# Kernel tuning notes

Measured on AMD Instinct MI355X. Metric: run time of the kernel, lower is better.

Reference implementation:

```python
import jax, jax.numpy as jnp
import numpy as np
import math

B, T, S, C, E = 8, 2048, 2048, 1024, 1024

def setup_inputs() -> dict:
    key = jax.random.key(0)
    ks = jax.random.split(key, 6)
    x = jax.random.normal(ks[0], (B, T, C), dtype=jnp.float32)
    tgt = jax.random.normal(ks[1], (B, T, E), dtype=jnp.float32)
    enc_a = jax.random.normal(ks[2], (B, E, S), dtype=jnp.float32)
    enc_b = jax.random.normal(ks[3], (B, S, E), dtype=jnp.float32)
    mask = jax.random.randint(ks[4], (B, S), 0, 2).astype(bool)
    w_in = jax.random.normal(ks[5], (E, C), dtype=jnp.float32) * math.sqrt(1.0 / C)
    b_in = jnp.zeros((E,), dtype=jnp.float32)
    w_out = jax.random.normal(jax.random.fold_in(key, 7), (C, E), dtype=jnp.float32) * math.sqrt(1.0 / E)
    b_out = jnp.zeros((C,), dtype=jnp.float32)
    return {"x": x, "target_embedding": tgt, "encoder_a": enc_a, "encoder_b": enc_b,
            "encoder_padding_mask": mask, "w_in": w_in, "b_in": b_in,
            "w_out": w_out, "b_out": b_out}

def reference(x, target_embedding, encoder_a, encoder_b, encoder_padding_mask,
              w_in, b_in, w_out, b_out):
    residual = x
    h = (jnp.einsum('btc,ec->bte', x, w_in) + b_in + target_embedding) * math.sqrt(0.5)
    # attention scores: [B, T, S]
    scores = jnp.einsum('bte,bes->bts', h, encoder_a)
    scores = jnp.where(encoder_padding_mask[:, None, :], -jnp.inf, scores)
    attn = jax.nn.softmax(scores, axis=-1)
    out = jnp.einsum('bts,bse->bte', attn, encoder_b)
    s = encoder_b.shape[1]
    out = out * (s * math.sqrt(1.0 / s))
    out = (jnp.einsum('bte,ce->btc', out, w_out) + b_out + residual) * math.sqrt(0.5)
    return (out, attn)
```

## Files before the change

kernel.cpp:

```cpp
#include <hip/hip_runtime.h>
#include <hip/hip_bf16.h>
#include <math.h>

#define NB 8
#define TT 2048
#define SS 2048
#define CC 1024
#define EE 1024
#define NMAX 1280

typedef __attribute__((ext_vector_type(8))) short short8;
typedef __attribute__((ext_vector_type(4))) float f32x4;

__device__ __forceinline__ unsigned short f2bf(float f) {
  unsigned u = __builtin_bit_cast(unsigned, f);
  u += 0x7fffu + ((u >> 16) & 1u);
  return (unsigned short)(u >> 16);
}
__device__ __forceinline__ float bf2f(unsigned short h) {
  unsigned u = ((unsigned)h) << 16;
  return __builtin_bit_cast(float, u);
}
__device__ __forceinline__ void gload16(const void* g, void* l) {
  __builtin_amdgcn_global_load_lds((const __attribute__((address_space(1))) void*)g,
                                   (__attribute__((address_space(3))) void*)l, 16, 0, 0);
}
__device__ __forceinline__ unsigned ldsoff(const void* p) {
  return (unsigned)(size_t)(const __attribute__((address_space(3))) char*)p;
}
__device__ __forceinline__ short8 ds128(unsigned off) {
  short8 r;
  asm volatile("ds_read_b128 %0, %1" : "=v"(r) : "v"(off));
  return r;
}
__device__ __forceinline__ int swzi(int x) { return x ^ (((x >> 7) & 7) << 4); }

#define WAITV(N) asm volatile("s_waitcnt vmcnt(" #N ")" ::: "memory")
#define WAITL(N) asm volatile("s_waitcnt lgkmcnt(" #N ")" ::: "memory")
#define BAR() __builtin_amdgcn_s_barrier()
#define SCH0() __builtin_amdgcn_sched_barrier(0)
#define PRIO1() __builtin_amdgcn_s_setprio(1)
#define PRIO0() __builtin_amdgcn_s_setprio(0)
#define MF(a_, b_, c_) __builtin_amdgcn_mfma_f32_16x16x32_bf16(a_, b_, c_, 0, 0, 0)

__device__ __forceinline__ int xcd_logical() {
  int gx = gridDim.x, gy = gridDim.y, gz = gridDim.z;
  int pid = blockIdx.x + gx * (blockIdx.y + gy * blockIdx.z);
  int q = (gx * gy * gz) >> 3;
  return (pid & 7) * q + (pid >> 3);
}

__global__ __launch_bounds__(256) void k_scan(const int* __restrict__ mask,
    int* __restrict__ idx, int* __restrict__ pfx, int* __restrict__ cnt,
    int* __restrict__ kpad) {
  __shared__ int cs[256];
  int b = blockIdx.x, t = threadIdx.x;
  const int* mrow = mask + (size_t)b * SS;
  int4 a = ((const int4*)mrow)[t * 2];
  int4 c2 = ((const int4*)mrow)[t * 2 + 1];
  int mm[8] = {a.x, a.y, a.z, a.w, c2.x, c2.y, c2.z, c2.w};
  int c = 0;
#pragma unroll
  for (int j = 0; j < 8; ++j) c += (mm[j] == 0);
  cs[t] = c;
  __syncthreads();
  if (t == 0) {
    int run = 0;
    for (int i = 0; i < 256; ++i) { int tmp = cs[i]; cs[i] = run; run += tmp; }
    cnt[b] = run;
    int kp = (run + 127) & ~127;
    if (kp > NMAX) kp = NMAX;
    kpad[b] = kp;
  }
  __syncthreads();
  int base = cs[t];
#pragma unroll
  for (int j = 0; j < 8; ++j) {
    int s = t * 8 + j;
    pfx[(size_t)b * SS + s] = base;
    if (mm[j] == 0) { idx[(size_t)b * SS + base] = s; base++; }
  }
}

__global__ __launch_bounds__(256) void k_split(const float* __restrict__ in,
    unsigned short* __restrict__ hi, unsigned short* __restrict__ lo, long n4) {
  long i = (long)blockIdx.x * blockDim.x + threadIdx.x;
  long stride = (long)gridDim.x * blockDim.x;
  for (; i < n4; i += stride) {
    float4 v = ((const float4*)in)[i];
    float f[4] = {v.x, v.y, v.z, v.w};
    unsigned short hh[4], ll[4];
#pragma unroll
    for (int j = 0; j < 4; ++j) {
      hh[j] = f2bf(f[j]);
      ll[j] = f2bf(f[j] - bf2f(hh[j]));
    }
    ushort4 h; h.x = hh[0]; h.y = hh[1]; h.z = hh[2]; h.w = hh[3];
    ushort4 l; l.x = ll[0]; l.y = ll[1]; l.z = ll[2]; l.w = ll[3];
    ((ushort4*)hi)[i] = h;
    ((ushort4*)lo)[i] = l;
  }
}

__global__ __launch_bounds__(256) void k_conv(const float* __restrict__ in,
    unsigned short* __restrict__ out, long n4) {
  long i = (long)blockIdx.x * blockDim.x + threadIdx.x;
  long stride = (long)gridDim.x * blockDim.x;
  for (; i < n4; i += stride) {
    float4 v = ((const float4*)in)[i];
    ushort4 h; h.x = f2bf(v.x); h.y = f2bf(v.y); h.z = f2bf(v.z); h.w = f2bf(v.w);
    ((ushort4*)out)[i] = h;
  }
}

__global__ __launch_bounds__(256) void k_ta(const float* __restrict__ enca,
    const int* __restrict__ idx, const int* __restrict__ cnt,
    unsigned short* __restrict__ hi, unsigned short* __restrict__ lo) {
  __shared__ float tile[64][65];
  int b = blockIdx.z, sc0 = blockIdx.x * 64, e0 = blockIdx.y * 64;
  int cb = cnt[b];
  const float* src = enca + (size_t)b * EE * SS;
  int t = threadIdx.x, tr = t >> 4, tc = (t & 15) * 4;
  int idxv[4];
#pragma unroll
  for (int j = 0; j < 4; ++j) {
    int sc = sc0 + tc + j;
    idxv[j] = (sc < cb) ? idx[(size_t)b * SS + sc] : -1;
  }
#pragma unroll
  for (int i = 0; i < 4; ++i) {
    int e = tr + i * 16;
#pragma unroll
    for (int j = 0; j < 4; ++j)
      tile[e][tc + j] = (idxv[j] >= 0) ? src[(size_t)(e0 + e) * SS + idxv[j]] : 0.f;
  }
  __syncthreads();
  size_t ob = (size_t)b * NMAX * EE;
#pragma unroll
  for (int i = 0; i < 4; ++i) {
    int c = tr + i * 16;
    unsigned short hh[4], ll[4];
#pragma unroll
    for (int j = 0; j < 4; ++j) {
      float f = tile[tc + j][c];
      hh[j] = f2bf(f);
      ll[j] = f2bf(f - bf2f(hh[j]));
    }
    ushort4 h; h.x = hh[0]; h.y = hh[1]; h.z = hh[2]; h.w = hh[3];
    ushort4 l; l.x = ll[0]; l.y = ll[1]; l.z = ll[2]; l.w = ll[3];
    *(ushort4*)(hi + ob + (size_t)(sc0 + c) * EE + e0 + tc) = h;
    *(ushort4*)(lo + ob + (size_t)(sc0 + c) * EE + e0 + tc) = l;
  }
}

__global__ __launch_bounds__(256) void k_tb(const float* __restrict__ encb,
    const int* __restrict__ idx, const int* __restrict__ cnt,
    unsigned short* __restrict__ out) {
  __shared__ float tile[64][65];
  int b = blockIdx.z, sc0 = blockIdx.x * 64, e0 = blockIdx.y * 64;
  int cb = cnt[b];
  const float* src = encb + (size_t)b * SS * EE;
  int t = threadIdx.x, tr = t >> 4, tc = (t & 15) * 4;
#pragma unroll
  for (int i = 0; i < 4; ++i) {
    int r = tr + i * 16;
    int sc = sc0 + r;
    int sidx = (sc < cb) ? idx[(size_t)b * SS + sc] : -1;
    float4 v;
    if (sidx >= 0) v = *(const float4*)(src + (size_t)sidx * EE + e0 + tc);
    else { v.x = v.y = v.z = v.w = 0.f; }
    tile[r][tc] = v.x; tile[r][tc + 1] = v.y; tile[r][tc + 2] = v.z; tile[r][tc + 3] = v.w;
  }
  __syncthreads();
  size_t ob = (size_t)b * EE * NMAX;
#pragma unroll
  for (int i = 0; i < 4; ++i) {
    int c = tr + i * 16;
    unsigned short hh[4];
#pragma unroll
    for (int j = 0; j < 4; ++j) hh[j] = f2bf(tile[tc + j][c]);
    ushort4 h; h.x = hh[0]; h.y = hh[1]; h.z = hh[2]; h.w = hh[3];
    *(ushort4*)(out + ob + (size_t)(e0 + c) * NMAX + sc0 + tc) = h;
  }
}

template <int EPI>
__global__ __launch_bounds__(512, 2) void k_gemm8(
    const unsigned short* __restrict__ A, const unsigned short* __restrict__ B,
    int N, int KROW, const int* __restrict__ kdyn, long sA, long sB, long sC,
    const float* __restrict__ bias, const float* __restrict__ addend,
    float* __restrict__ outF, unsigned short* __restrict__ outH, float scale) {
  extern __shared__ char lds[];
  const int tid = threadIdx.x, wave = tid >> 6, lane = tid & 63;
  int L = xcd_logical();
  const int n0 = (L % gridDim.x) * 256;
  int tmpL = L / gridDim.x;
  const int m0 = (tmpL % gridDim.y) * 256;
  const int b = tmpL / gridDim.y;
  const int KD = kdyn ? kdyn[b] : KROW;
  const int wm = wave >> 2, wn = wave & 3;
  const unsigned short* gA = A + (size_t)b * sA + (size_t)m0 * KROW;
  const unsigned short* gB = B + (size_t)b * sB + (size_t)n0 * KROW;
  const unsigned ldsB = ldsoff(lds);

  int srow[2], sk8[2];
#pragma unroll
  for (int s = 0; s < 2; ++s) {
    int l = swzi((s * 512 + tid) * 16);
    srow[s] = l >> 6;
    sk8[s] = (l >> 4) & 3;
  }
  const int aR = wm * 128 + (lane & 15);
  const int bR = wn * 64 + (lane & 15);
  const int kB = (lane >> 4) * 16;
  const int nkt = KD >> 6;

  f32x4 acc[8][4] = {};

  auto STG = [&](int t, int tensor, int ks) {
    const unsigned short* g = tensor ? gB : gA;
    char* dst = lds + (t & 1) * 65536 + tensor * 32768 + ks * 16384 + wave * 1024;
    size_t gk = (size_t)t * 64 + ks * 32;
#pragma unroll
    for (int s = 0; s < 2; ++s)
      gload16(g + ((size_t)srow[s] * KROW + gk + sk8[s] * 8), dst + s * 8192);
  };
  auto RA = [&](int t, int ks, int mf) {
    int lin = (aR + mf * 16) * 64 + kB;
    return ds128(ldsB + (t & 1) * 65536 + ks * 16384 + swzi(lin));
  };
  auto RB = [&](int t, int ks, int nf) {
    int lin = (bR + nf * 16) * 64 + kB;
    return ds128(ldsB + (t & 1) * 65536 + 32768 + ks * 16384 + swzi(lin));
  };

  STG(0, 1, 0); STG(0, 0, 0); STG(0, 0, 1); STG(0, 1, 1);
  if (nkt > 1) { STG(1, 1, 0); STG(1, 0, 0); }

  for (int u = 0; u < nkt; ++u) {
    if (u + 1 < nkt) { WAITV(8); } else { WAITV(0); }
    BAR();
    short8 bf[4], af[4];
#pragma unroll
    for (int nf = 0; nf < 4; ++nf) bf[nf] = RB(u, 0, nf);
#pragma unroll
    for (int mf = 0; mf < 4; ++mf) af[mf] = RA(u, 0, mf);
    if (u + 1 < nkt) { STG(u + 1, 0, 1); STG(u + 1, 1, 1); }
    BAR(); WAITL(0); SCH0(); PRIO1();
#pragma unroll
    for (int mf = 0; mf < 4; ++mf)
#pragma unroll
      for (int nf = 0; nf < 4; ++nf) acc[mf][nf] = MF(af[mf], bf[nf], acc[mf][nf]);
    PRIO0(); SCH0(); BAR();
#pragma unroll
    for (int mf = 0; mf < 4; ++mf) af[mf] = RA(u, 0, mf + 4);
    if (u + 2 < nkt) STG(u + 2, 1, 0);
    BAR(); WAITL(0); SCH0(); PRIO1();
#pragma unroll
    for (int mf = 0; mf < 4; ++mf)
#pragma unroll
      for (int nf = 0; nf < 4; ++nf) acc[mf + 4][nf] = MF(af[mf], bf[nf], acc[mf + 4][nf]);
    PRIO0(); SCH0();
    if (u + 2 < nkt) { WAITV(10); } else if (u + 1 < nkt) { WAITV(8); } else { WAITV(0); }
    BAR();
#pragma unroll
    for (int nf = 0; nf < 4; ++nf) bf[nf] = RB(u, 1, nf);
#pragma unroll
    for (int mf = 0; mf < 4; ++mf) af[mf] = RA(u, 1, mf);
    if (u + 2 < nkt) STG(u + 2, 0, 0);
    BAR(); WAITL(0); SCH0(); PRIO1();
#pragma unroll
    for (int mf = 0; mf < 4; ++mf)
#pragma unroll
      for (int nf = 0; nf < 4; ++nf) acc[mf][nf] = MF(af[mf], bf[nf], acc[mf][nf]);
    PRIO0(); SCH0(); BAR();
#pragma unroll
    for (int mf = 0; mf < 4; ++mf) af[mf] = RA(u, 1, mf + 4);
    BAR(); WAITL(0); SCH0(); PRIO1();
#pragma unroll
    for (int mf = 0; mf < 4; ++mf)
#pragma unroll
      for (int nf = 0; nf < 4; ++nf) acc[mf + 4][nf] = MF(af[mf], bf[nf], acc[mf + 4][nf]);
    PRIO0(); SCH0(); BAR();
  }

  const size_t cb = (size_t)b * sC;
  const int mB = m0 + wm * 128 + ((lane >> 4) << 2);
  const int nB = n0 + wn * 64 + (lane & 15);
#pragma unroll
  for (int mf = 0; mf < 8; ++mf)
#pragma unroll
    for (int j = 0; j < 4; ++j) {
      int m = mB + mf * 16 + j;
#pragma unroll
      for (int nf = 0; nf < 4; ++nf) {
        int n = nB + nf * 16;
        float v = acc[mf][nf][j];
        size_t o = (size_t)m * N + n;
        if (EPI == 2) outH[cb + o] = f2bf(v * scale);
        else outF[o] = (v + bias[n] + addend[o]) * scale;
      }
    }
}

template <int EPI>
__global__ __launch_bounds__(512, 2) void k_split8(
    const unsigned short* __restrict__ Ah, const unsigned short* __restrict__ Al,
    const unsigned short* __restrict__ Bh, const unsigned short* __restrict__ Bl,
    int N, int K, long sA, long sB, long sC,
    const float* __restrict__ bias, const float* __restrict__ addend,
    float* __restrict__ outF, unsigned short* __restrict__ outHi,
    unsigned short* __restrict__ outLo, float scale, const int* __restrict__ npad) {
  extern __shared__ char lds[];
  const int tid = threadIdx.x, wave = tid >> 6, lane = tid & 63;
  int L = xcd_logical();
  const int n0 = (L % gridDim.x) * 128;
  int tmpL = L / gridDim.x;
  const int m0 = (tmpL % gridDim.y) * 256;
  const int b = tmpL / gridDim.y;
  if (npad && n0 >= npad[b]) return;
  const int wm = wave >> 1, wn = wave & 1;
  const unsigned short* gAh = Ah + (size_t)b * sA + (size_t)m0 * K;
  const unsigned short* gAl = Al + (size_t)b * sA + (size_t)m0 * K;
  const unsigned short* gBh = Bh + (size_t)b * sB + (size_t)n0 * K;
  const unsigned short* gBl = Bl + (size_t)b * sB + (size_t)n0 * K;
  const unsigned ldsB = ldsoff(lds);

  int aoff[2], boff;
#pragma unroll
  for (int s = 0; s < 2; ++s) {
    int l = swzi((s * 512 + tid) * 16);
    aoff[s] = (l >> 6) * K + ((l >> 4) & 3) * 8;
  }
  { int l = swzi(tid * 16); boff = (l >> 6) * K + ((l >> 4) & 3) * 8; }
  const int aR = wm * 64 + (lane & 15);
  const int bR = wn * 64 + (lane & 15);
  const int kB = (lane >> 4) * 16;
  const int nkt = K >> 5;

  const unsigned vA = ldsB + (unsigned)swzi(aR * 64 + kB);
  const unsigned vB = ldsB + 32768u + (unsigned)swzi(bR * 64 + kB);

  f32x4 acc[4][4] = {};

  auto STG_A = [&](int t, int bb, int hilo) {
    char* dst = lds + bb * 49152 + hilo * 16384 + tid * 16;
    const unsigned short* g = (hilo ? gAl : gAh) + (size_t)t * 32;
    gload16(g + aoff[0], dst);
    gload16(g + aoff[1], dst + 8192);
  };
  auto STG_B = [&](int t, int bb, int hilo) {
    char* dst = lds + bb * 49152 + 32768 + hilo * 8192 + tid * 16;
    const unsigned short* g = (hilo ? gBl : gBh) + (size_t)t * 32;
    gload16(g + boff, dst);
  };

  STG_A(0, 0, 0); STG_B(0, 0, 0); STG_B(0, 0, 1); STG_A(0, 0, 1);
  STG_A(1, 1, 0); STG_B(1, 1, 0); STG_B(1, 1, 1); STG_A(1, 1, 1);

  int bc = 0;
  for (int u = 0; u < nkt; ++u) {
    int bs = bc + 2; if (bs >= 3) bs -= 3;
    const unsigned cb_ = bc * 49152u;
    short8 ahi[4], bhi[4], xf[4];
    if (u + 1 < nkt) { WAITV(6); } else { WAITV(0); }
    BAR();
#pragma unroll
    for (int q = 0; q < 4; ++q) bhi[q] = ds128(vB + cb_ + q * 1024);
#pragma unroll
    for (int q = 0; q < 4; ++q) ahi[q] = ds128(vA + cb_ + q * 1024);
    if (u + 2 < nkt) { STG_A(u + 2, bs, 0); STG_B(u + 2, bs, 0); }
    BAR(); WAITL(0); SCH0(); PRIO1();
#pragma unroll
    for (int mi = 0; mi < 4; ++mi)
#pragma unroll
      for (int ni = 0; ni < 4; ++ni) acc[mi][ni] = MF(ahi[mi], bhi[ni], acc[mi][ni]);
    PRIO0(); SCH0();
    BAR();
#pragma unroll
    for (int q = 0; q < 4; ++q) xf[q] = ds128(vB + cb_ + 8192 + q * 1024);
    if (u + 2 < nkt) { STG_B(u + 2, bs, 1); STG_A(u + 2, bs, 1); }
    BAR(); WAITL(0); SCH0(); PRIO1();
#pragma unroll
    for (int mi = 0; mi < 4; ++mi)
#pragma unroll
      for (int ni = 0; ni < 4; ++ni) acc[mi][ni] = MF(ahi[mi], xf[ni], acc[mi][ni]);
    PRIO0(); SCH0();
    BAR();
#pragma unroll
    for (int q = 0; q < 4; ++q) xf[q] = ds128(vA + cb_ + 16384 + q * 1024);
    BAR(); WAITL(0); SCH0(); PRIO1();
#pragma unroll
    for (int mi = 0; mi < 4; ++mi)
#pragma unroll
      for (int ni = 0; ni < 4; ++ni) acc[mi][ni] = MF(xf[mi], bhi[ni], acc[mi][ni]);
    PRIO0(); SCH0();
    bc = bc + 1; if (bc >= 3) bc -= 3;
  }

  const size_t cb = (size_t)b * sC;
  const int mB = m0 + wm * 64 + ((lane >> 4) << 2);
  const int nB = n0 + wn * 64 + (lane & 15);
#pragma unroll
  for (int mf = 0; mf < 4; ++mf)
#pragma unroll
    for (int j = 0; j < 4; ++j) {
      int m = mB + mf * 16 + j;
#pragma unroll
      for (int nf = 0; nf < 4; ++nf) {
        int n = nB + nf * 16;
        float v = acc[mf][nf][j];
        size_t o = (size_t)m * N + n;
        if (EPI == 0) {
          v = (v + bias[n] + addend[o]) * scale;
          unsigned short hb = f2bf(v);
          outHi[o] = hb;
          outLo[o] = f2bf(v - bf2f(hb));
        } else {
          outF[cb + o] = v;
        }
      }
    }
}

__global__ __launch_bounds__(256) void k_softmax(const float* __restrict__ scores_c,
    float* __restrict__ attn, unsigned short* __restrict__ attn_bc,
    const int* __restrict__ mask, const int* __restrict__ pfx,
    const int* __restrict__ cnt, const int* __restrict__ kpad) {
  __shared__ float sl[NMAX];
  __shared__ float red[8];
  long r = blockIdx.x;
  int b = (int)(r >> 11);
  int t = threadIdx.x;
  int cb = cnt[b], kp = kpad[b];
  const float* srow = scores_c + r * (long)NMAX;
  for (int i = t; i < cb; i += 256) sl[i] = srow[i];
  __syncthreads();
  int base = t * 8;
  const int* mrow = mask + (size_t)b * SS;
  int4 m0i = *(const int4*)(mrow + base);
  int4 m1i = *(const int4*)(mrow + base + 4);
  int mm[8] = {m0i.x, m0i.y, m0i.z, m0i.w, m1i.x, m1i.y, m1i.z, m1i.w};
  const int* prow = pfx + (size_t)b * SS;
  int4 p0i = *(const int4*)(prow + base);
  int4 p1i = *(const int4*)(prow + base + 4);
  int pp[8] = {p0i.x, p0i.y, p0i.z, p0i.w, p1i.x, p1i.y, p1i.z, p1i.w};
  float v[8];
#pragma unroll
  for (int j = 0; j < 8; ++j) v[j] = mm[j] ? -INFINITY : sl[pp[j]];
  float mx = v[0];
#pragma unroll
  for (int j = 1; j < 8; ++j) mx = fmaxf(mx, v[j]);
#pragma unroll
  for (int off = 32; off; off >>= 1) mx = fmaxf(mx, __shfl_xor(mx, off));
  int wv = t >> 6, ln = t & 63;
  if (ln == 0) red[wv] = mx;
  __syncthreads();
  mx = fmaxf(fmaxf(red[0], red[1]), fmaxf(red[2], red[3]));
  float sum = 0.f;
#pragma unroll
  for (int j = 0; j < 8; ++j) { v[j] = __expf(v[j] - mx); sum += v[j]; }
#pragma unroll
  for (int off = 32; off; off >>= 1) sum += __shfl_xor(sum, off);
  if (ln == 0) red[4 + wv] = sum;
  __syncthreads();
  sum = (red[4] + red[5]) + (red[6] + red[7]);
  float inv = 1.0f / sum;
#pragma unroll
  for (int j = 0; j < 8; ++j) v[j] *= inv;
  float* arow = attn + r * (long)SS;
  float4 w0; w0.x = v[0]; w0.y = v[1]; w0.z = v[2]; w0.w = v[3];
  float4 w1; w1.x = v[4]; w1.y = v[5]; w1.z = v[6]; w1.w = v[7];
  *(float4*)(arow + base) = w0;
  *(float4*)(arow + base + 4) = w1;
  __syncthreads();
#pragma unroll
  for (int j = 0; j < 8; ++j) if (!mm[j]) sl[pp[j]] = v[j];
  __syncthreads();
  unsigned short* brow = attn_bc + r * (long)NMAX;
  for (int i = t; i < kp; i += 256) brow[i] = f2bf(i < cb ? sl[i] : 0.f);
}

extern "C" void kernel_launch(void* const* d_in, const int* in_sizes, int n_in,
                              void* d_out, int out_size, void* d_ws, size_t ws_size,
                              hipStream_t stream) {
  (void)in_sizes; (void)n_in; (void)out_size; (void)ws_size;
  const float* x     = (const float*)d_in[0];
  const float* tgt   = (const float*)d_in[1];
  const float* enca  = (const float*)d_in[2];
  const float* encb  = (const float*)d_in[3];
  const int*   mask  = (const int*)d_in[4];
  const float* w_in  = (const float*)d_in[5];
  const float* b_in  = (const float*)d_in[6];
  const float* w_out = (const float*)d_in[7];
  const float* b_out = (const float*)d_in[8];

  float* out  = (float*)d_out;
  float* attn = out + (size_t)NB * TT * CC;

  char* ws = (char*)d_ws;
  float*          scores_c = (float*)(ws + 0);
  unsigned short* x_hi   = (unsigned short*)(ws + 0);
  unsigned short* x_lo   = (unsigned short*)(ws + 33554432L);
  unsigned short* pv     = (unsigned short*)(ws + 0);
  unsigned short* h_hi   = (unsigned short*)(ws + 83886080L);
  unsigned short* h_lo   = (unsigned short*)(ws + 117440512L);
  unsigned short* attn_bc= (unsigned short*)(ws + 83886080L);
  unsigned short* a_tc_hi= (unsigned short*)(ws + 150994944L);
  unsigned short* a_tc_lo= (unsigned short*)(ws + 171966464L);
  unsigned short* b_tc   = (unsigned short*)(ws + 192937984L);
  unsigned short* w_in_hi= (unsigned short*)(ws + 213909504L);
  unsigned short* w_in_lo= (unsigned short*)(ws + 216006656L);
  unsigned short* w_out_b= (unsigned short*)(ws + 218103808L);
  int* idx  = (int*)(ws + 220200960L);
  int* pfx  = (int*)(ws + 220266496L);
  int* cnt  = (int*)(ws + 220332032L);
  int* kpad = (int*)(ws + 220332096L);

  hipFuncSetAttribute(reinterpret_cast<const void*>(&k_gemm8<2>),
                      hipFuncAttributeMaxDynamicSharedMemorySize, 131072);
  hipFuncSetAttribute(reinterpret_cast<const void*>(&k_gemm8<3>),
                      hipFuncAttributeMaxDynamicSharedMemorySize, 131072);
  hipFuncSetAttribute(reinterpret_cast<const void*>(&k_split8<0>),
                      hipFuncAttributeMaxDynamicSharedMemorySize, 147456);
  hipFuncSetAttribute(reinterpret_cast<const void*>(&k_split8<1>),
                      hipFuncAttributeMaxDynamicSharedMemorySize, 147456);

  dim3 blk(256), blk512(512);
  const float S05 = 0.70710678118654752f;

  k_scan<<<NB, blk, 0, stream>>>(mask, idx, pfx, cnt, kpad);
  k_split<<<2048, blk, 0, stream>>>(x, x_hi, x_lo, (long)NB * TT * CC / 4);
  k_split<<<512, blk, 0, stream>>>(w_in, w_in_hi, w_in_lo, (long)EE * CC / 4);
  k_conv<<<512, blk, 0, stream>>>(w_out, w_out_b, (long)CC * EE / 4);
  k_ta<<<dim3(NMAX / 64, EE / 64, NB), blk, 0, stream>>>(enca, idx, cnt, a_tc_hi, a_tc_lo);
  k_tb<<<dim3(NMAX / 64, EE / 64, NB), blk, 0, stream>>>(encb, idx, cnt, b_tc);

  k_split8<0><<<dim3(EE / 128, (NB * TT) / 256, 1), blk512, 147456, stream>>>(
      x_hi, x_lo, w_in_hi, w_in_lo, EE, CC, 0, 0, 0,
      b_in, tgt, nullptr, h_hi, h_lo, S05, nullptr);

  k_split8<1><<<dim3(NMAX / 128, TT / 256, NB), blk512, 147456, stream>>>(
      h_hi, h_lo, a_tc_hi, a_tc_lo, NMAX, EE,
      (long)TT * EE, (long)NMAX * EE, (long)TT * NMAX,
      nullptr, nullptr, scores_c, nullptr, nullptr, 1.0f, kpad);

  k_softmax<<<NB * TT, blk, 0, stream>>>(scores_c, attn, attn_bc, mask, pfx, cnt, kpad);

  k_gemm8<2><<<dim3(EE / 256, TT / 256, NB), blk512, 131072, stream>>>(
      attn_bc, b_tc, EE, NMAX, kpad,
      (long)TT * NMAX, (long)EE * NMAX, (long)TT * EE,
      nullptr, nullptr, nullptr, pv, 45.254833995939045f);

  k_gemm8<3><<<dim3(CC / 256, (NB * TT) / 256, 1), blk512, 131072, stream>>>(
      pv, w_out_b, CC, EE, nullptr, 0, 0, 0,
      b_out, x, out, nullptr, S05);
}
```

Measured before the change: 516.0 us.

## Enlarge split-bf16 GEMM tile to 256x256 with double-buffered six-phase pipeline

The split-precision GEMM kernel now computes 256x256 output tiles instead of 256x128. Waves are arranged 2x4, each holding 8x4 accumulators. The previous triple-buffered LDS ring becomes a double buffer of 64KB stages, with each K-step split into six MFMA phases that interleave staging of the four hi/lo operand regions. The goal is higher arithmetic intensity and fewer global loads per FLOP. The cost is more accumulator registers and fewer blocks; for the scores GEMM, coarser N tiles also mean the padding skip (n0 >= npad) discards work less precisely.

```diff
diff --git a/kernel.cpp b/kernel.cpp
--- a/kernel.cpp
+++ b/kernel.cpp
@@ -314,95 +314,122 @@
   extern __shared__ char lds[];
   const int tid = threadIdx.x, wave = tid >> 6, lane = tid & 63;
   int L = xcd_logical();
-  const int n0 = (L % gridDim.x) * 128;
+  const int n0 = (L % gridDim.x) * 256;
   int tmpL = L / gridDim.x;
   const int m0 = (tmpL % gridDim.y) * 256;
   const int b = tmpL / gridDim.y;
   if (npad && n0 >= npad[b]) return;
-  const int wm = wave >> 1, wn = wave & 1;
-  const unsigned short* gAh = Ah + (size_t)b * sA + (size_t)m0 * K;
-  const unsigned short* gAl = Al + (size_t)b * sA + (size_t)m0 * K;
-  const unsigned short* gBh = Bh + (size_t)b * sB + (size_t)n0 * K;
-  const unsigned short* gBl = Bl + (size_t)b * sB + (size_t)n0 * K;
+  const int wm = wave >> 2, wn = wave & 3;
+  const unsigned short* gb[4];
+  gb[0] = Ah + (size_t)b * sA + (size_t)m0 * K;
+  gb[1] = Al + (size_t)b * sA + (size_t)m0 * K;
+  gb[2] = Bh + (size_t)b * sB + (size_t)n0 * K;
+  gb[3] = Bl + (size_t)b * sB + (size_t)n0 * K;
   const unsigned ldsB = ldsoff(lds);
 
-  int aoff[2], boff;
+  int soff[2];
 #pragma unroll
   for (int s = 0; s < 2; ++s) {
     int l = swzi((s * 512 + tid) * 16);
-    aoff[s] = (l >> 6) * K + ((l >> 4) & 3) * 8;
-  }
-  { int l = swzi(tid * 16); boff = (l >> 6) * K + ((l >> 4) & 3) * 8; }
-  const int aR = wm * 64 + (lane & 15);
+    soff[s] = (l >> 6) * K + ((l >> 4) & 3) * 8;
+  }
+  const int aR = wm * 128 + (lane & 15);
   const int bR = wn * 64 + (lane & 15);
   const int kB = (lane >> 4) * 16;
   const int nkt = K >> 5;
 
-  const unsigned vA = ldsB + (unsigned)swzi(aR * 64 + kB);
-  const unsigned vB = ldsB + 32768u + (unsigned)swzi(bR * 64 + kB);
-
-  f32x4 acc[4][4] = {};
-
-  auto STG_A = [&](int t, int bb, int hilo) {
-    char* dst = lds + bb * 49152 + hilo * 16384 + tid * 16;
-    const unsigned short* g = (hilo ? gAl : gAh) + (size_t)t * 32;
-    gload16(g + aoff[0], dst);
-    gload16(g + aoff[1], dst + 8192);
+  unsigned vA = ldsB + (unsigned)swzi(aR * 64 + kB);
+  unsigned vB = ldsB + (unsigned)swzi(bR * 64 + kB);
+
+  f32x4 acc[8][4] = {};
+
+  auto STG2 = [&](int t, unsigned bufbase, int region) {
+    char* dst = lds + bufbase + region * 16384 + tid * 16;
+    const unsigned short* g = gb[region] + (size_t)t * 32;
+#pragma unroll
+    for (int s = 0; s < 2; ++s)
+      gload16(g + soff[s], dst + s * 8192);
   };
-  auto STG_B = [&](int t, int bb, int hilo) {
-    char* dst = lds + bb * 49152 + 32768 + hilo * 8192 + tid * 16;
-    const unsigned short* g = (hilo ? gBl : gBh) + (size_t)t * 32;
-    gload16(g + boff, dst);
-  };
-
-  STG_A(0, 0, 0); STG_B(0, 0, 0); STG_B(0, 0, 1); STG_A(0, 0, 1);
-  STG_A(1, 1, 0); STG_B(1, 1, 0); STG_B(1, 1, 1); STG_A(1, 1, 1);
-
-  int bc = 0;
-  for (int u = 0; u < nkt; ++u) {
-    int bs = bc + 2; if (bs >= 3) bs -= 3;
-    const unsigned cb_ = bc * 49152u;
-    short8 ahi[4], bhi[4], xf[4];
-    if (u + 1 < nkt) { WAITV(6); } else { WAITV(0); }
-    BAR();
-#pragma unroll
-    for (int q = 0; q < 4; ++q) bhi[q] = ds128(vB + cb_ + q * 1024);
-#pragma unroll
-    for (int q = 0; q < 4; ++q) ahi[q] = ds128(vA + cb_ + q * 1024);
-    if (u + 2 < nkt) { STG_A(u + 2, bs, 0); STG_B(u + 2, bs, 0); }
-    BAR(); WAITL(0); SCH0(); PRIO1();
-#pragma unroll
-    for (int mi = 0; mi < 4; ++mi)
-#pragma unroll
-      for (int ni = 0; ni < 4; ++ni) acc[mi][ni] = MF(ahi[mi], bhi[ni], acc[mi][ni]);
-    PRIO0(); SCH0();
-    BAR();
-#pragma unroll
-    for (int q = 0; q < 4; ++q) xf[q] = ds128(vB + cb_ + 8192 + q * 1024);
-    if (u + 2 < nkt) { STG_B(u + 2, bs, 1); STG_A(u + 2, bs, 1); }
-    BAR(); WAITL(0); SCH0(); PRIO1();
-#pragma unroll
-    for (int mi = 0; mi < 4; ++mi)
-#pragma unroll
-      for (int ni = 0; ni < 4; ++ni) acc[mi][ni] = MF(ahi[mi], xf[ni], acc[mi][ni]);
-    PRIO0(); SCH0();
-    BAR();
-#pragma unroll
-    for (int q = 0; q < 4; ++q) xf[q] = ds128(vA + cb_ + 16384 + q * 1024);
-    BAR(); WAITL(0); SCH0(); PRIO1();
-#pragma unroll
-    for (int mi = 0; mi < 4; ++mi)
-#pragma unroll
-      for (int ni = 0; ni < 4; ++ni) acc[mi][ni] = MF(xf[mi], bhi[ni], acc[mi][ni]);
-    PRIO0(); SCH0();
-    bc = bc + 1; if (bc >= 3) bc -= 3;
-  }
+
+#define PH_TOP() BAR()
+#define PH_MID() BAR(); WAITL(0); SCH0(); PRIO1()
+#define PH_END() PRIO0(); SCH0()
+
+#define TILE(u, WV1, WV3, WV5, STAGE) do {                                     \
+  short8 ahi[8], bhi[4], blo[4], alo[4];                                       \
+                                                         \
+  WV1; PH_TOP();                                                               \
+  _Pragma("unroll") for (int q = 0; q < 4; ++q) bhi[q] = ds128(vB + 32768 + q * 1024); \
+  _Pragma("unroll") for (int q = 0; q < 4; ++q) ahi[q] = ds128(vA + q * 1024); \
+  if (STAGE) STG2((u) + 1, nbuf, 0);                                           \
+  PH_MID();                                                                    \
+  _Pragma("unroll") for (int mi = 0; mi < 4; ++mi)                             \
+  _Pragma("unroll") for (int ni = 0; ni < 4; ++ni)                             \
+    acc[mi][ni] = MF(ahi[mi], bhi[ni], acc[mi][ni]);                           \
+  PH_END();                                                                    \
+                                                         \
+  PH_TOP();                                                                    \
+  _Pragma("unroll") for (int q = 0; q < 4; ++q) ahi[4 + q] = ds128(vA + (4 + q) * 1024); \
+  if (STAGE) STG2((u) + 1, nbuf, 2);                                           \
+  PH_MID();                                                                    \
+  _Pragma("unroll") for (int mi = 0; mi < 4; ++mi)                             \
+  _Pragma("unroll") for (int ni = 0; ni < 4; ++ni)                             \
+    acc[4 + mi][ni] = MF(ahi[4 + mi], bhi[ni], acc[4 + mi][ni]);               \
+  PH_END();                                                                    \
+                                                         \
+  WV3; PH_TOP();                                                               \
+  _Pragma("unroll") for (int q = 0; q < 4; ++q) blo[q] = ds128(vB + 49152 + q * 1024); \
+  if (STAGE) STG2((u) + 1, nbuf, 3);                                           \
+  PH_MID();                                                                    \
+  _Pragma("unroll") for (int mi = 0; mi < 4; ++mi)                             \
+  _Pragma("unroll") for (int ni = 0; ni < 4; ++ni)                             \
+    acc[mi][ni] = MF(ahi[mi], blo[ni], acc[mi][ni]);                           \
+  PH_END();                                                                    \
+                                                         \
+  PH_TOP();                                                                    \
+  if (STAGE) STG2((u) + 1, nbuf, 1);                                           \
+  PH_MID();                                                                    \
+  _Pragma("unroll") for (int mi = 0; mi < 4; ++mi)                             \
+  _Pragma("unroll") for (int ni = 0; ni < 4; ++ni)                             \
+    acc[4 + mi][ni] = MF(ahi[4 + mi], blo[ni], acc[4 + mi][ni]);               \
+  PH_END();                                                                    \
+                                                         \
+  WV5; PH_TOP();                                                               \
+  _Pragma("unroll") for (int q = 0; q < 4; ++q) alo[q] = ds128(vA + 16384 + q * 1024); \
+  PH_MID();                                                                    \
+  _Pragma("unroll") for (int mi = 0; mi < 4; ++mi)                             \
+  _Pragma("unroll") for (int ni = 0; ni < 4; ++ni)                             \
+    acc[mi][ni] = MF(alo[mi], bhi[ni], acc[mi][ni]);                           \
+  PH_END();                                                                    \
+                                                         \
+  PH_TOP();                                                                    \
+  _Pragma("unroll") for (int q = 0; q < 4; ++q) alo[q] = ds128(vA + 16384 + (4 + q) * 1024); \
+  PH_MID();                                                                    \
+  _Pragma("unroll") for (int mi = 0; mi < 4; ++mi)                             \
+  _Pragma("unroll") for (int ni = 0; ni < 4; ++ni)                             \
+    acc[4 + mi][ni] = MF(alo[mi], bhi[ni], acc[4 + mi][ni]);                   \
+  PH_END();                                                                    \
+  vA ^= 65536u; vB ^= 65536u;                                                  \
+} while (0)
+
+  STG2(0, 0, 0); STG2(0, 0, 2); STG2(0, 0, 3); STG2(0, 0, 1);
+
+  unsigned nbuf = 65536u;
+  for (int u = 0; u < nkt - 1; ++u) {
+    TILE(u, WAITV(4), WAITV(6), WAITV(8), 1);
+    nbuf ^= 65536u;
+  }
+  TILE(nkt - 1, WAITV(4), WAITV(2), WAITV(0), 0);
+#undef TILE
+#undef PH_TOP
+#undef PH_MID
+#undef PH_END
 
   const size_t cb = (size_t)b * sC;
-  const int mB = m0 + wm * 64 + ((lane >> 4) << 2);
+  const int mB = m0 + wm * 128 + ((lane >> 4) << 2);
   const int nB = n0 + wn * 64 + (lane & 15);
 #pragma unroll
-  for (int mf = 0; mf < 4; ++mf)
+  for (int mf = 0; mf < 8; ++mf)
 #pragma unroll
     for (int j = 0; j < 4; ++j) {
       int m = mB + mf * 16 + j;
@@ -522,9 +549,9 @@
   hipFuncSetAttribute(reinterpret_cast<const void*>(&k_gemm8<3>),
                       hipFuncAttributeMaxDynamicSharedMemorySize, 131072);
   hipFuncSetAttribute(reinterpret_cast<const void*>(&k_split8<0>),
-                      hipFuncAttributeMaxDynamicSharedMemorySize, 147456);
+                      hipFuncAttributeMaxDynamicSharedMemorySize, 131072);
   hipFuncSetAttribute(reinterpret_cast<const void*>(&k_split8<1>),
-                      hipFuncAttributeMaxDynamicSharedMemorySize, 147456);
+                      hipFuncAttributeMaxDynamicSharedMemorySize, 131072);
 
   dim3 blk(256), blk512(512);
   const float S05 = 0.70710678118654752f;
@@ -536,11 +563,11 @@
   k_ta<<<dim3(NMAX / 64, EE / 64, NB), blk, 0, stream>>>(enca, idx, cnt, a_tc_hi, a_tc_lo);
   k_tb<<<dim3(NMAX / 64, EE / 64, NB), blk, 0, stream>>>(encb, idx, cnt, b_tc);
 
-  k_split8<0><<<dim3(EE / 128, (NB * TT) / 256, 1), blk512, 147456, stream>>>(
+  k_split8<0><<<dim3(EE / 256, (NB * TT) / 256, 1), blk512, 131072, stream>>>(
       x_hi, x_lo, w_in_hi, w_in_lo, EE, CC, 0, 0, 0,
       b_in, tgt, nullptr, h_hi, h_lo, S05, nullptr);
 
-  k_split8<1><<<dim3(NMAX / 128, TT / 256, NB), blk512, 147456, stream>>>(
+  k_split8<1><<<dim3(NMAX / 256, TT / 256, NB), blk512, 131072, stream>>>(
       h_hi, h_lo, a_tc_hi, a_tc_lo, NMAX, EE,
       (long)TT * EE, (long)NMAX * EE, (long)TT * NMAX,
       nullptr, nullptr, scores_c, nullptr, nullptr, 1.0f, kpad);
```

New measurement: 511.1 us. Within noise of the previous version (-0.9%).
